# Kernel optimization log

Hardware: AMD Instinct MI355X
Metric: run time of the kernel (lower is better)

## Reference

```python
import jax, jax.numpy as jnp
import numpy as np


def setup_inputs() -> dict:
    key = jax.random.key(0)
    x = jax.random.normal(key, (32, 80, 3000), dtype=jnp.float32)
    return {"x": x, "left_frames": 5, "right_frames": 5}


def reference(x, left_frames, right_frames):
    # Faithful to the torch grouped conv1d with an identity-pattern kernel:
    # out channel (f, c) at time t equals x[f, t + c + lag - P] with zero padding,
    # where P = max(l, r), lag = r - l if r > l else 0, context_len = l + r + 1.
    B, F, T = x.shape
    P = max(left_frames, right_frames)
    lag = right_frames - left_frames if right_frames > left_frames else 0
    context_len = left_frames + right_frames + 1
    xp = jnp.pad(x, ((0, 0), (0, 0), (P, P)))  # zero padding on time axis
    # Stack shifted slices: [B, F, context_len, T]; small static loop over context.
    frames = jnp.stack(
        [xp[..., c + lag : c + lag + T] for c in range(context_len)], axis=2
    )
    # Channel layout matches kernel.repeat(F,1,1).view(F*context_len, ...):
    # output channel index = f * context_len + c
    return frames.reshape(B, F * context_len, T)
```

## Files before the change

### kernel.cpp

```cpp
#include <hip/hip_runtime.h>


#define BB   32
#define FF   80
#define TT   3000
#define PW   5
#define CTX  11
#define T4   (TT / 4)
#define NTHREADS 256
#define NJJ  3

typedef float vf4 __attribute__((ext_vector_type(4)));

__global__ __launch_bounds__(NTHREADS) void context_window_43233140801616_kernel(
    const float* __restrict__ x, float* __restrict__ out) {
    __shared__ vf4 s4buf[(TT + 2 * PW + 2) / 4 + 1];
    float* s = (float*)s4buf;
    const vf4* s4 = (const vf4*)s;

    const int row = blockIdx.x;
    const int tid = threadIdx.x;

    const vf4* xrow = (const vf4*)(x + (size_t)row * TT);
    for (int j = tid; j < T4; j += NTHREADS) {
        vf4 v = xrow[j];
        int base = PW + 4 * j;
        s[base + 0] = v.x;
        s[base + 1] = v.y;
        s[base + 2] = v.z;
        s[base + 3] = v.w;
    }
    if (tid < PW) {
        s[tid] = 0.0f;
        s[TT + PW + tid] = 0.0f;
    }
    if (tid < 6) {
        s[TT + 2 * PW + tid] = 0.0f;
    }
    __syncthreads();

    float w[NJJ][16];
#pragma unroll
    for (int jj = 0; jj < NJJ; ++jj) {
        int j = tid + jj * NTHREADS;
        if (j < T4) {
            vf4 a = s4[j];
            vf4 b = s4[j + 1];
            vf4 c4 = s4[j + 2];
            vf4 d = s4[j + 3];
            w[jj][0] = a.x;  w[jj][1] = a.y;  w[jj][2] = a.z;  w[jj][3] = a.w;
            w[jj][4] = b.x;  w[jj][5] = b.y;  w[jj][6] = b.z;  w[jj][7] = b.w;
            w[jj][8] = c4.x; w[jj][9] = c4.y; w[jj][10] = c4.z; w[jj][11] = c4.w;
            w[jj][12] = d.x; w[jj][13] = d.y; w[jj][14] = d.z; w[jj][15] = d.w;
        }
    }

    float* orow = out + (size_t)row * CTX * TT;
#pragma unroll
    for (int c = 0; c < CTX; ++c) {
        vf4* oc = (vf4*)(orow + c * TT);
#pragma unroll
        for (int jj = 0; jj < NJJ; ++jj) {
            int j = tid + jj * NTHREADS;
            if (j < T4) {
                vf4 v = {w[jj][c], w[jj][c + 1], w[jj][c + 2], w[jj][c + 3]};
                oc[j] = v;
            }
        }
    }
}

extern "C" void kernel_launch(void* const* d_in, const int* in_sizes, int n_in,
                              void* d_out, int out_size, void* d_ws, size_t ws_size,
                              hipStream_t stream) {
    const float* x = (const float*)d_in[0];
    float* out = (float*)d_out;
    context_window_43233140801616_kernel<<<BB * FF, NTHREADS, 0, stream>>>(x, out);
}
```

Before: 362.5 us.

## Replace shared-memory row staging with grid-stride per-output vector gathers

Drops the per-row LDS staging, the barrier, and the register window. Each thread now walks the flattened output in float4 units with a grid-stride loop over a fixed number of blocks. It rebuilds row, context and time indices with integer divisions and reads input directly from global memory, usually as unaligned vector loads, and zero-fills values at the borders. The aim is to make the write stream fully flat and contiguous. The cost is the index arithmetic per element and about 11x redundant input reads, which are expected to hit in cache, plus possibly unaligned global loads.

```diff
diff --git a/kernel.cpp b/kernel.cpp
--- a/kernel.cpp
+++ b/kernel.cpp
@@ -7,66 +7,40 @@
 #define PW   5
 #define CTX  11
 #define T4   (TT / 4)
+#define ROWS (BB * FF)
+#define ROWF4 (CTX * T4)
+#define TOTALF4 (ROWS * ROWF4)
 #define NTHREADS 256
-#define NJJ  3
+#define NBLOCKS  2048
 
 typedef float vf4 __attribute__((ext_vector_type(4)));
 
 __global__ __launch_bounds__(NTHREADS) void context_window_43233140801616_kernel(
     const float* __restrict__ x, float* __restrict__ out) {
-    __shared__ vf4 s4buf[(TT + 2 * PW + 2) / 4 + 1];
-    float* s = (float*)s4buf;
-    const vf4* s4 = (const vf4*)s;
+    const unsigned stride = NBLOCKS * NTHREADS;
+    vf4* __restrict__ out4 = (vf4*)out;
 
-    const int row = blockIdx.x;
-    const int tid = threadIdx.x;
+    for (unsigned i = blockIdx.x * NTHREADS + threadIdx.x; i < TOTALF4;
+         i += stride) {
+        unsigned row = i / ROWF4;
+        unsigned rem = i - row * ROWF4;
+        unsigned c   = rem / T4;
+        unsigned t4  = rem - c * T4;
 
-    const vf4* xrow = (const vf4*)(x + (size_t)row * TT);
-    for (int j = tid; j < T4; j += NTHREADS) {
-        vf4 v = xrow[j];
-        int base = PW + 4 * j;
-        s[base + 0] = v.x;
-        s[base + 1] = v.y;
-        s[base + 2] = v.z;
-        s[base + 3] = v.w;
-    }
-    if (tid < PW) {
-        s[tid] = 0.0f;
-        s[TT + PW + tid] = 0.0f;
-    }
-    if (tid < 6) {
-        s[TT + 2 * PW + tid] = 0.0f;
-    }
-    __syncthreads();
+        const float* xrow = x + (size_t)row * TT;
+        int start = (int)(4u * t4 + c) - PW;
 
-    float w[NJJ][16];
+        vf4 v;
+        if (start >= 0 && start + 3 < TT) {
+            __builtin_memcpy(&v, xrow + start, sizeof(vf4));
+        } else {
 #pragma unroll
-    for (int jj = 0; jj < NJJ; ++jj) {
-        int j = tid + jj * NTHREADS;
-        if (j < T4) {
-            vf4 a = s4[j];
-            vf4 b = s4[j + 1];
-            vf4 c4 = s4[j + 2];
-            vf4 d = s4[j + 3];
-            w[jj][0] = a.x;  w[jj][1] = a.y;  w[jj][2] = a.z;  w[jj][3] = a.w;
-            w[jj][4] = b.x;  w[jj][5] = b.y;  w[jj][6] = b.z;  w[jj][7] = b.w;
-            w[jj][8] = c4.x; w[jj][9] = c4.y; w[jj][10] = c4.z; w[jj][11] = c4.w;
-            w[jj][12] = d.x; w[jj][13] = d.y; w[jj][14] = d.z; w[jj][15] = d.w;
-        }
-    }
-
-    float* orow = out + (size_t)row * CTX * TT;
-#pragma unroll
-    for (int c = 0; c < CTX; ++c) {
-        vf4* oc = (vf4*)(orow + c * TT);
-#pragma unroll
-        for (int jj = 0; jj < NJJ; ++jj) {
-            int j = tid + jj * NTHREADS;
-            if (j < T4) {
-                vf4 v = {w[jj][c], w[jj][c + 1], w[jj][c + 2], w[jj][c + 3]};
-                oc[j] = v;
+            for (int k = 0; k < 4; ++k) {
+                int idx = start + k;
+                v[k] = (idx >= 0 && idx < TT) ? xrow[idx] : 0.0f;
             }
         }
+        out4[i] = v;
     }
 }
 
@@ -75,5 +49,5 @@
                               hipStream_t stream) {
     const float* x = (const float*)d_in[0];
     float* out = (float*)d_out;
-    context_window_43233140801616_kernel<<<BB * FF, NTHREADS, 0, stream>>>(x, out);
+    context_window_43233140801616_kernel<<<NBLOCKS, NTHREADS, 0, stream>>>(x, out);
 }
```

Measured after the change: 399.3 us. 10.1% more time.

## Process five rows per block with register prefetch of next input row

Applied to the files above, without the earlier changes.

Each block now handles five consecutive rows instead of one, and the grid drops from 2560 blocks to 512. The next row's input is prefetched into registers before the current row's output stores are issued. The aim is to overlap input load latency with output writes and to cut block launch overhead. The cost is fewer blocks for latency hiding and an extra barrier per row.

```diff
diff --git a/kernel.cpp b/kernel.cpp
--- a/kernel.cpp
+++ b/kernel.cpp
@@ -9,6 +9,8 @@
 #define T4   (TT / 4)
 #define NTHREADS 256
 #define NJJ  3
+#define NBLOCKS 512
+#define RPB  5
 
 typedef float vf4 __attribute__((ext_vector_type(4)));
 
@@ -18,53 +20,79 @@
     float* s = (float*)s4buf;
     const vf4* s4 = (const vf4*)s;
 
-    const int row = blockIdx.x;
     const int tid = threadIdx.x;
+    const int row0 = blockIdx.x * RPB;
 
-    const vf4* xrow = (const vf4*)(x + (size_t)row * TT);
-    for (int j = tid; j < T4; j += NTHREADS) {
-        vf4 v = xrow[j];
-        int base = PW + 4 * j;
-        s[base + 0] = v.x;
-        s[base + 1] = v.y;
-        s[base + 2] = v.z;
-        s[base + 3] = v.w;
-    }
-    if (tid < PW) {
-        s[tid] = 0.0f;
-        s[TT + PW + tid] = 0.0f;
-    }
-    if (tid < 6) {
-        s[TT + 2 * PW + tid] = 0.0f;
-    }
-    __syncthreads();
-
-    float w[NJJ][16];
+    vf4 pf[NJJ];
+    {
+        const vf4* xrow = (const vf4*)(x + (size_t)row0 * TT);
 #pragma unroll
-    for (int jj = 0; jj < NJJ; ++jj) {
-        int j = tid + jj * NTHREADS;
-        if (j < T4) {
-            vf4 a = s4[j];
-            vf4 b = s4[j + 1];
-            vf4 c4 = s4[j + 2];
-            vf4 d = s4[j + 3];
-            w[jj][0] = a.x;  w[jj][1] = a.y;  w[jj][2] = a.z;  w[jj][3] = a.w;
-            w[jj][4] = b.x;  w[jj][5] = b.y;  w[jj][6] = b.z;  w[jj][7] = b.w;
-            w[jj][8] = c4.x; w[jj][9] = c4.y; w[jj][10] = c4.z; w[jj][11] = c4.w;
-            w[jj][12] = d.x; w[jj][13] = d.y; w[jj][14] = d.z; w[jj][15] = d.w;
+        for (int jj = 0; jj < NJJ; ++jj) {
+            int j = tid + jj * NTHREADS;
+            if (j < T4) pf[jj] = xrow[j];
         }
     }
 
-    float* orow = out + (size_t)row * CTX * TT;
-#pragma unroll
-    for (int c = 0; c < CTX; ++c) {
-        vf4* oc = (vf4*)(orow + c * TT);
+    for (int r = 0; r < RPB; ++r) {
+        const int row = row0 + r;
+
 #pragma unroll
         for (int jj = 0; jj < NJJ; ++jj) {
             int j = tid + jj * NTHREADS;
             if (j < T4) {
-                vf4 v = {w[jj][c], w[jj][c + 1], w[jj][c + 2], w[jj][c + 3]};
-                oc[j] = v;
+                int base = PW + 4 * j;
+                s[base + 0] = pf[jj].x;
+                s[base + 1] = pf[jj].y;
+                s[base + 2] = pf[jj].z;
+                s[base + 3] = pf[jj].w;
+            }
+        }
+        if (tid < PW) {
+            s[tid] = 0.0f;
+            s[TT + PW + tid] = 0.0f;
+        }
+        if (tid < 6) {
+            s[TT + 2 * PW + tid] = 0.0f;
+        }
+        __syncthreads();
+
+        float w[NJJ][16];
+#pragma unroll
+        for (int jj = 0; jj < NJJ; ++jj) {
+            int j = tid + jj * NTHREADS;
+            if (j < T4) {
+                vf4 a = s4[j];
+                vf4 b = s4[j + 1];
+                vf4 c4 = s4[j + 2];
+                vf4 d = s4[j + 3];
+                w[jj][0] = a.x;  w[jj][1] = a.y;  w[jj][2] = a.z;  w[jj][3] = a.w;
+                w[jj][4] = b.x;  w[jj][5] = b.y;  w[jj][6] = b.z;  w[jj][7] = b.w;
+                w[jj][8] = c4.x; w[jj][9] = c4.y; w[jj][10] = c4.z; w[jj][11] = c4.w;
+                w[jj][12] = d.x; w[jj][13] = d.y; w[jj][14] = d.z; w[jj][15] = d.w;
+            }
+        }
+        __syncthreads();
+
+        if (r + 1 < RPB) {
+            const vf4* xrow = (const vf4*)(x + (size_t)(row + 1) * TT);
+#pragma unroll
+            for (int jj = 0; jj < NJJ; ++jj) {
+                int j = tid + jj * NTHREADS;
+                if (j < T4) pf[jj] = xrow[j];
+            }
+        }
+
+        float* orow = out + (size_t)row * CTX * TT;
+#pragma unroll
+        for (int c = 0; c < CTX; ++c) {
+            vf4* oc = (vf4*)(orow + c * TT);
+#pragma unroll
+            for (int jj = 0; jj < NJJ; ++jj) {
+                int j = tid + jj * NTHREADS;
+                if (j < T4) {
+                    vf4 v = {w[jj][c], w[jj][c + 1], w[jj][c + 2], w[jj][c + 3]};
+                    oc[j] = v;
+                }
             }
         }
     }
@@ -75,5 +103,5 @@
                               hipStream_t stream) {
     const float* x = (const float*)d_in[0];
     float* out = (float*)d_out;
-    context_window_43233140801616_kernel<<<BB * FF, NTHREADS, 0, stream>>>(x, out);
+    context_window_43233140801616_kernel<<<NBLOCKS, NTHREADS, 0, stream>>>(x, out);
 }
```

New measurement: 367.4 us. No clear change (+1.3%).
